# Kernel tuning notes

Hardware: AMD Instinct MI355X
Metric: run time of the kernel (lower is better)

The kernel has to match this reference:

```python
import jax, jax.numpy as jnp
import numpy as np

SEARCH_RANGE = 4


def setup_inputs() -> dict:
    key = jax.random.key(0)
    k1, k2 = jax.random.split(key)
    B, C, H, W = 4, 64, 256, 256
    x1 = jax.random.normal(k1, (B, C, H, W), dtype=jnp.float32)
    x2 = jax.random.normal(k2, (B, C, H, W), dtype=jnp.float32)
    return {"x1": x1, "x2": x2}


def reference(x1, x2):
    r = SEARCH_RANGE
    D = (2 * r + 1) ** 2
    B, C, H, W = x1.shape
    # zero-pad x2 so out-of-range correlations contribute 0 (matches the
    # original, which leaves those cv entries at their zero init)
    x2p = jnp.pad(x2, ((0, 0), (0, 0), (r, r), (r, r)))
    chans = [None] * D
    for i in range(-r, r + 1):
        for j in range(-r, r + 1):
            # torch cv[:, (2r+1)*i + j] wraps negative indices -> mod D
            k = ((2 * r + 1) * i + j) % D
            # x2 sample at (h - i, w - j): window of padded x2
            win = jax.lax.dynamic_slice(
                x2p, (0, 0, r - i, r - j), (B, C, H, W))
            chans[k] = jnp.sum(x1 * win, axis=1)  # [B,H,W]
    cv = jnp.stack(chans, axis=1)  # [B,D,H,W]
    return jax.nn.softmax(cv, axis=1)  # alpha=1, raw_output=False
```

## Files before the change

### kernel.cpp

```cpp
#include <hip/hip_runtime.h>
#include <stddef.h>

namespace {
constexpr int Hc = 256, Wc = 256, Cc = 64, Bc = 4, Dc = 81;
constexpr int CH = Hc * Wc;
}

#define PIN() asm volatile("" ::: "memory")
#define VMW(N) asm volatile("s_waitcnt vmcnt(" #N ")" ::: "memory")

#define GLOAD_LDS16(g, l)                                                   \
    __builtin_amdgcn_global_load_lds(                                       \
        (const __attribute__((address_space(1))) void*)(g),                 \
        (__attribute__((address_space(3))) void*)(l), 16, 0, 0)

#define DPPL(x) __builtin_amdgcn_update_dpp(0, (x), 0x138, 0xf, 0xf, true)
#define DPPR(x) __builtin_amdgcn_update_dpp(0, (x), 0x130, 0xf, 0xf, true)

#define FMAS(P, A, Bv, Cv)                                                  \
    do {                                                                    \
        const float w_[12] = {A.x,  A.y,  A.z,  A.w,  Bv.x, Bv.y,           \
                              Bv.z, Bv.w, Cv.x, Cv.y, Cv.z, Cv.w};          \
        const float pv_[4] = {P.x, P.y, P.z, P.w};                          \
        _Pragma("unroll") for (int jj = 0; jj < 9; ++jj)                    \
            _Pragma("unroll") for (int s = 0; s < 4; ++s)                   \
                acc[jj][s] += pv_[s] * w_[s - jj + 8];                      \
    } while (0)

#define FM(S, P)                                                            \
    do {                                                                    \
        const int b0_ = __float_as_int(xq##S.x);                            \
        const int b1_ = __float_as_int(xq##S.y);                            \
        const int b2_ = __float_as_int(xq##S.z);                            \
        const int b3_ = __float_as_int(xq##S.w);                            \
        float4 L_, R_;                                                      \
        L_.x = __int_as_float(DPPL(b0_)); L_.y = __int_as_float(DPPL(b1_)); \
        L_.z = __int_as_float(DPPL(b2_)); L_.w = __int_as_float(DPPL(b3_)); \
        R_.x = __int_as_float(DPPR(b0_)); R_.y = __int_as_float(DPPR(b1_)); \
        R_.z = __int_as_float(DPPR(b2_)); R_.w = __int_as_float(DPPR(b3_)); \
        FMAS(P, L_, xq##S, R_);                                             \
    } while (0)

#define RD1(N, RP) N = *(const float4*)(RP)
#define ISX(T, OFF)                                                         \
    do {                                                                    \
        xq##T = *(const float4*)(x2p + (size_t)(OFF) * CH);                 \
        PIN();                                                              \
    } while (0)

#define GROUPN(CUR, NXT)                                                    \
    do {                                                                    \
        GLOAD_LDS16(x1g + (size_t)(8 + mwi) * CH, (NXT) + wi * 256);        \
        PIN();                                                              \
        RD1(xb, (CUR) + 1 * 256 + 4 * t); VMW(8); FM(0, xa); ISX(0, 8);     \
        RD1(xa, (CUR) + 2 * 256 + 4 * t); VMW(8); FM(1, xb); ISX(1, 9);     \
        RD1(xb, (CUR) + 3 * 256 + 4 * t); VMW(8); FM(2, xa); ISX(2, 10);    \
        RD1(xa, (CUR) + 4 * 256 + 4 * t); VMW(8); FM(3, xb); ISX(3, 11);    \
        RD1(xb, (CUR) + 5 * 256 + 4 * t); VMW(8); FM(4, xa); ISX(4, 12);    \
        RD1(xa, (CUR) + 6 * 256 + 4 * t); VMW(8); FM(5, xb); ISX(5, 13);    \
        RD1(xb, (CUR) + 7 * 256 + 4 * t); VMW(8); FM(6, xa); ISX(6, 14);    \
        VMW(8); FM(7, xb); ISX(7, 15);                                      \
        VMW(8);                                                             \
        PIN(); __builtin_amdgcn_s_barrier(); PIN();                         \
        RD1(xa, (NXT) + 4 * t);                                             \
        x2p += (size_t)8 * CH; x1g += (size_t)8 * CH;                       \
    } while (0)

__global__ __launch_bounds__(576)
void corr_softmax_kernel(const float* __restrict__ x1,
                         const float* __restrict__ x2,
                         float* __restrict__ out)
{
    __shared__ __align__(16) float bufA[9 * 256];
    __shared__ __align__(16) float bufB[9 * 256];

    const int tid = threadIdx.x;
    const int wi  = tid >> 6;
    const int t   = tid & 63;
    const int mwi = (wi < 8) ? wi : 7;
    const int bid = blockIdx.x;
    const int bh  = (bid & 7) * 128 + (bid >> 3);
    const int b   = bh >> 8;
    const int h   = bh & 255;

    float acc[9][4];
#pragma unroll
    for (int jj = 0; jj < 9; ++jj)
#pragma unroll
        for (int s = 0; s < 4; ++s)
            acc[jj][s] = 0.f;

    const int r  = h + 4 - wi;
    const int rr = (r < 0) ? 0 : ((r > 255) ? 255 : r);

    const float* x2p = x2 + (size_t)b * Cc * CH + (size_t)rr * Wc + 4 * t;
    const float* x1g = x1 + (size_t)b * Cc * CH + (size_t)h * Wc + 4 * t;

    float4 xq0, xq1, xq2, xq3, xq4, xq5, xq6, xq7, xa, xb;

    GLOAD_LDS16(x1g + (size_t)mwi * CH, bufA + wi * 256);
    PIN();
    ISX(0, 0); ISX(1, 1); ISX(2, 2); ISX(3, 3);
    ISX(4, 4); ISX(5, 5); ISX(6, 6); ISX(7, 7);
    VMW(8);
    PIN(); __builtin_amdgcn_s_barrier(); PIN();
    RD1(xa, bufA + 4 * t);

#pragma unroll 1
    for (int g = 0; g < 3; ++g) {
        GROUPN(bufA, bufB);
        GROUPN(bufB, bufA);
    }
    GROUPN(bufA, bufB);

    RD1(xb, bufB + 1 * 256 + 4 * t); VMW(7); FM(0, xa);
    RD1(xa, bufB + 2 * 256 + 4 * t); VMW(6); FM(1, xb);
    RD1(xb, bufB + 3 * 256 + 4 * t); VMW(5); FM(2, xa);
    RD1(xa, bufB + 4 * 256 + 4 * t); VMW(4); FM(3, xb);
    RD1(xb, bufB + 5 * 256 + 4 * t); VMW(3); FM(4, xa);
    RD1(xa, bufB + 6 * 256 + 4 * t); VMW(2); FM(5, xb);
    RD1(xb, bufB + 7 * 256 + 4 * t); VMW(1); FM(6, xa);
    VMW(0); FM(7, xb);

    if ((unsigned)r >= (unsigned)Hc) {
#pragma unroll
        for (int jj = 0; jj < 9; ++jj)
#pragma unroll
            for (int s = 0; s < 4; ++s)
                acc[jj][s] = 0.f;
    }

    __syncthreads();
    float* red = bufA;

    float m0, m1, m2, m3;
    {
        float v0 = acc[0][0], v1 = acc[0][1], v2 = acc[0][2], v3 = acc[0][3];
#pragma unroll
        for (int jj = 1; jj < 9; ++jj) {
            v0 = fmaxf(v0, acc[jj][0]);
            v1 = fmaxf(v1, acc[jj][1]);
            v2 = fmaxf(v2, acc[jj][2]);
            v3 = fmaxf(v3, acc[jj][3]);
        }
        m0 = v0; m1 = v1; m2 = v2; m3 = v3;
    }
    *(float4*)(red + wi * 256 + 4 * t) = make_float4(m0, m1, m2, m3);
    __syncthreads();

    float M0, M1, M2, M3;
    {
        float4 q = *(const float4*)(red + 4 * t);
        M0 = q.x; M1 = q.y; M2 = q.z; M3 = q.w;
#pragma unroll
        for (int w2 = 1; w2 < 9; ++w2) {
            float4 qq = *(const float4*)(red + w2 * 256 + 4 * t);
            M0 = fmaxf(M0, qq.x); M1 = fmaxf(M1, qq.y);
            M2 = fmaxf(M2, qq.z); M3 = fmaxf(M3, qq.w);
        }
    }

    float s0 = 0.f, s1 = 0.f, s2 = 0.f, s3 = 0.f;
#pragma unroll
    for (int jj = 0; jj < 9; ++jj) {
        acc[jj][0] = __expf(acc[jj][0] - M0); s0 += acc[jj][0];
        acc[jj][1] = __expf(acc[jj][1] - M1); s1 += acc[jj][1];
        acc[jj][2] = __expf(acc[jj][2] - M2); s2 += acc[jj][2];
        acc[jj][3] = __expf(acc[jj][3] - M3); s3 += acc[jj][3];
    }
    __syncthreads();
    *(float4*)(red + wi * 256 + 4 * t) = make_float4(s0, s1, s2, s3);
    __syncthreads();

    float S0, S1, S2, S3;
    {
        float4 q = *(const float4*)(red + 4 * t);
        S0 = q.x; S1 = q.y; S2 = q.z; S3 = q.w;
#pragma unroll
        for (int w2 = 1; w2 < 9; ++w2) {
            float4 qq = *(const float4*)(red + w2 * 256 + 4 * t);
            S0 += qq.x; S1 += qq.y; S2 += qq.z; S3 += qq.w;
        }
    }
    const float i0 = 1.0f / S0, i1 = 1.0f / S1, i2 = 1.0f / S2, i3 = 1.0f / S3;

    float* outp = out + (size_t)b * Dc * CH + (size_t)h * Wc + 4 * t;
#pragma unroll
    for (int jj = 0; jj < 9; ++jj) {
        int kc = 9 * wi + jj + 41;
        if (kc >= 81) kc -= 81;
        float4 o = make_float4(acc[jj][0] * i0, acc[jj][1] * i1,
                               acc[jj][2] * i2, acc[jj][3] * i3);
        *(float4*)(outp + (size_t)kc * CH) = o;
    }
}

extern "C" void kernel_launch(void* const* d_in, const int* in_sizes, int n_in,
                              void* d_out, int out_size, void* d_ws, size_t ws_size,
                              hipStream_t stream) {
    (void)in_sizes; (void)n_in; (void)d_ws; (void)ws_size; (void)out_size;
    const float* x1 = (const float*)d_in[0];
    const float* x2 = (const float*)d_in[1];
    float* out = (float*)d_out;
    dim3 grid(Bc * Hc);
    dim3 block(576);
    hipLaunchKernelGGL(corr_softmax_kernel, grid, block, 0, stream, x1, x2, out);
}
```

Baseline: 82.27 us.

## Pack channel pairs to fp16 and accumulate correlations with fdot2

Converts pairs of channels of x1 and x2 into packed half2 values and accumulates the 81 correlations with v_dot2 fp32-accumulate instructions, halving the FMA count and the DPP shuffle count. The x2 prefetch pipeline is restructured to keep 4 float4 registers in flight instead of 8, with adjusted waitcnt depths and paired LDS reads. This lowers compute and register pressure but drops input precision to fp16 (round-toward-zero), which may exceed the tolerance, and the shallower prefetch may expose more memory latency.

```diff
diff --git a/kernel.cpp b/kernel.cpp
--- a/kernel.cpp
+++ b/kernel.cpp
@@ -17,52 +17,68 @@
 #define DPPL(x) __builtin_amdgcn_update_dpp(0, (x), 0x138, 0xf, 0xf, true)
 #define DPPR(x) __builtin_amdgcn_update_dpp(0, (x), 0x130, 0xf, 0xf, true)
 
-#define FMAS(P, A, Bv, Cv)                                                  \
-    do {                                                                    \
-        const float w_[12] = {A.x,  A.y,  A.z,  A.w,  Bv.x, Bv.y,           \
-                              Bv.z, Bv.w, Cv.x, Cv.y, Cv.z, Cv.w};          \
-        const float pv_[4] = {P.x, P.y, P.z, P.w};                          \
+typedef __fp16 half2v __attribute__((ext_vector_type(2)));
+
+static __device__ __forceinline__ int pk2(float a, float b) {
+#if __has_builtin(__builtin_amdgcn_cvt_pkrtz)
+    half2v h = __builtin_amdgcn_cvt_pkrtz(a, b);
+#else
+    half2v h; h.x = (__fp16)a; h.y = (__fp16)b;
+#endif
+    return __builtin_bit_cast(int, h);
+}
+
+static __device__ __forceinline__ float dot2f(int q, int w, float c) {
+#if __has_builtin(__builtin_amdgcn_fdot2)
+    return __builtin_amdgcn_fdot2(__builtin_bit_cast(half2v, q),
+                                  __builtin_bit_cast(half2v, w), c, false);
+#else
+    half2v a = __builtin_bit_cast(half2v, q);
+    half2v b = __builtin_bit_cast(half2v, w);
+    return c + (float)a.x * (float)b.x + (float)a.y * (float)b.y;
+#endif
+}
+
+#define FMP(A0, A1, X0, X1)                                                 \
+    do {                                                                    \
+        const int P0_ = pk2(A0.x, A1.x), P1_ = pk2(A0.y, A1.y);             \
+        const int P2_ = pk2(A0.z, A1.z), P3_ = pk2(A0.w, A1.w);             \
+        const int w_[12] = {DPPL(P0_), DPPL(P1_), DPPL(P2_), DPPL(P3_),     \
+                            P0_,       P1_,       P2_,       P3_,           \
+                            DPPR(P0_), DPPR(P1_), DPPR(P2_), DPPR(P3_)};    \
+        const int q_[4] = {pk2(X0.x, X1.x), pk2(X0.y, X1.y),                \
+                           pk2(X0.z, X1.z), pk2(X0.w, X1.w)};               \
         _Pragma("unroll") for (int jj = 0; jj < 9; ++jj)                    \
             _Pragma("unroll") for (int s = 0; s < 4; ++s)                   \
-                acc[jj][s] += pv_[s] * w_[s - jj + 8];                      \
-    } while (0)
-
-#define FM(S, P)                                                            \
-    do {                                                                    \
-        const int b0_ = __float_as_int(xq##S.x);                            \
-        const int b1_ = __float_as_int(xq##S.y);                            \
-        const int b2_ = __float_as_int(xq##S.z);                            \
-        const int b3_ = __float_as_int(xq##S.w);                            \
-        float4 L_, R_;                                                      \
-        L_.x = __int_as_float(DPPL(b0_)); L_.y = __int_as_float(DPPL(b1_)); \
-        L_.z = __int_as_float(DPPL(b2_)); L_.w = __int_as_float(DPPL(b3_)); \
-        R_.x = __int_as_float(DPPR(b0_)); R_.y = __int_as_float(DPPR(b1_)); \
-        R_.z = __int_as_float(DPPR(b2_)); R_.w = __int_as_float(DPPR(b3_)); \
-        FMAS(P, L_, xq##S, R_);                                             \
-    } while (0)
-
-#define RD1(N, RP) N = *(const float4*)(RP)
+                acc[jj][s] = dot2f(q_[s], w_[s - jj + 8], acc[jj][s]);      \
+    } while (0)
+
 #define ISX(T, OFF)                                                         \
     do {                                                                    \
         xq##T = *(const float4*)(x2p + (size_t)(OFF) * CH);                 \
         PIN();                                                              \
     } while (0)
 
+#define RDX1(N0, N1, RA, RB, SLAB)                                          \
+    do {                                                                    \
+        N0 = *(const float4*)((SLAB) + (RA) * 256 + 4 * t);                 \
+        N1 = *(const float4*)((SLAB) + (RB) * 256 + 4 * t);                 \
+    } while (0)
+
 #define GROUPN(CUR, NXT)                                                    \
     do {                                                                    \
         GLOAD_LDS16(x1g + (size_t)(8 + mwi) * CH, (NXT) + wi * 256);        \
         PIN();                                                              \
-        RD1(xb, (CUR) + 1 * 256 + 4 * t); VMW(8); FM(0, xa); ISX(0, 8);     \
-        RD1(xa, (CUR) + 2 * 256 + 4 * t); VMW(8); FM(1, xb); ISX(1, 9);     \
-        RD1(xb, (CUR) + 3 * 256 + 4 * t); VMW(8); FM(2, xa); ISX(2, 10);    \
-        RD1(xa, (CUR) + 4 * 256 + 4 * t); VMW(8); FM(3, xb); ISX(3, 11);    \
-        RD1(xb, (CUR) + 5 * 256 + 4 * t); VMW(8); FM(4, xa); ISX(4, 12);    \
-        RD1(xa, (CUR) + 6 * 256 + 4 * t); VMW(8); FM(5, xb); ISX(5, 13);    \
-        RD1(xb, (CUR) + 7 * 256 + 4 * t); VMW(8); FM(6, xa); ISX(6, 14);    \
-        VMW(8); FM(7, xb); ISX(7, 15);                                      \
-        VMW(8);                                                             \
+        RDX1(xn0, xn1, 2, 3, CUR); VMW(3); FMP(xq0, xq1, xc0, xc1);         \
+        ISX(0, 4); ISX(1, 5);                                               \
+        RDX1(xc0, xc1, 4, 5, CUR); VMW(3); FMP(xq2, xq3, xn0, xn1);         \
+        ISX(2, 6); ISX(3, 7);                                               \
+        RDX1(xn0, xn1, 6, 7, CUR); VMW(2); FMP(xq0, xq1, xc0, xc1);         \
+        ISX(0, 8); ISX(1, 9);                                               \
+        VMW(2); FMP(xq2, xq3, xn0, xn1);                                    \
+        ISX(2, 10); ISX(3, 11);                                             \
         PIN(); __builtin_amdgcn_s_barrier(); PIN();                         \
-        RD1(xa, (NXT) + 4 * t);                                             \
+        RDX1(xc0, xc1, 0, 1, NXT);                                          \
         x2p += (size_t)8 * CH; x1g += (size_t)8 * CH;                       \
     } while (0)
 
@@ -96,15 +112,15 @@
     const float* x2p = x2 + (size_t)b * Cc * CH + (size_t)rr * Wc + 4 * t;
     const float* x1g = x1 + (size_t)b * Cc * CH + (size_t)h * Wc + 4 * t;
 
-    float4 xq0, xq1, xq2, xq3, xq4, xq5, xq6, xq7, xa, xb;
+    float4 xq0, xq1, xq2, xq3;
+    float4 xc0, xc1, xn0, xn1;
 
     GLOAD_LDS16(x1g + (size_t)mwi * CH, bufA + wi * 256);
     PIN();
     ISX(0, 0); ISX(1, 1); ISX(2, 2); ISX(3, 3);
-    ISX(4, 4); ISX(5, 5); ISX(6, 6); ISX(7, 7);
-    VMW(8);
+    VMW(4);
     PIN(); __builtin_amdgcn_s_barrier(); PIN();
-    RD1(xa, bufA + 4 * t);
+    RDX1(xc0, xc1, 0, 1, bufA);
 
 #pragma unroll 1
     for (int g = 0; g < 3; ++g) {
@@ -113,14 +129,12 @@
     }
     GROUPN(bufA, bufB);
 
-    RD1(xb, bufB + 1 * 256 + 4 * t); VMW(7); FM(0, xa);
-    RD1(xa, bufB + 2 * 256 + 4 * t); VMW(6); FM(1, xb);
-    RD1(xb, bufB + 3 * 256 + 4 * t); VMW(5); FM(2, xa);
-    RD1(xa, bufB + 4 * 256 + 4 * t); VMW(4); FM(3, xb);
-    RD1(xb, bufB + 5 * 256 + 4 * t); VMW(3); FM(4, xa);
-    RD1(xa, bufB + 6 * 256 + 4 * t); VMW(2); FM(5, xb);
-    RD1(xb, bufB + 7 * 256 + 4 * t); VMW(1); FM(6, xa);
-    VMW(0); FM(7, xb);
+    RDX1(xn0, xn1, 2, 3, bufB); VMW(2); FMP(xq0, xq1, xc0, xc1);
+    ISX(0, 4); ISX(1, 5);
+    RDX1(xc0, xc1, 4, 5, bufB); VMW(2); FMP(xq2, xq3, xn0, xn1);
+    ISX(2, 6); ISX(3, 7);
+    RDX1(xn0, xn1, 6, 7, bufB); VMW(2); FMP(xq0, xq1, xc0, xc1);
+    VMW(0); FMP(xq2, xq3, xn0, xn1);
 
     if ((unsigned)r >= (unsigned)Hc) {
 #pragma unroll
```

Measured after the change: 70.53 us. 14.3% less time.
